# Kernel optimization log

Hardware: AMD Instinct MI355X
Metric: run time of the kernel (lower is better)

## Reference

```python
import jax, jax.numpy as jnp
import numpy as np
from jax import lax


def _shifted(X, k, alpha):
    # alpha * roll(X, -k, 0) + (1 - alpha) * roll(X, -k-1, 0), via gather
    N = X.shape[0]
    idx = (jnp.arange(N) + k) % N
    return alpha * X[idx] + (1.0 - alpha) * X[(idx + 1) % N]


def _all_distances(D_q, D_p, steps):
    # steps: [S] float32 signed step values. Returns [S] mean L2 distances.
    N = D_q.shape[0]
    rows = jnp.arange(N)

    def dist_one(step):
        s = jnp.abs(step)
        k = jnp.floor(s).astype(jnp.int32)          # int(step) of |step|
        alpha = s - k.astype(step.dtype)
        diff = lax.cond(
            step >= 0,
            lambda: _shifted(D_q, k, alpha) - D_p,   # shift query forward
            lambda: D_q - _shifted(D_p, k, alpha),   # shift positive (ref) forward
        )
        norms = jnp.sqrt(jnp.sum(diff * diff, axis=-1))  # [N]
        valid = rows < (N - k)                       # rows [:N - int_step]
        return jnp.sum(jnp.where(valid, norms, 0.0)) / (N - k).astype(norms.dtype)

    def body(carry, step):
        return carry, dist_one(step)

    _, dists = lax.scan(body, None, steps)
    return dists


def setup_inputs() -> dict:
    key = jax.random.key(0)
    k1, k2 = jax.random.split(key)
    N, D = 100000, 256
    return {
        "D_q": jax.random.normal(k1, (N, D), dtype=jnp.float32),
        "D_p": jax.random.normal(k2, (N, D), dtype=jnp.float32),
        "max_step": 60,
        "step_size": 1,
    }


def reference(D_q, D_p, max_step, step_size):
    # Same candidate step schedule as the torch loop (static, built on host).
    steps_np = np.concatenate([
        np.arange(0, max_step, step_size),
        -np.arange(1, max_step + 1, step_size),
    ]).astype(np.float32)
    steps = jnp.asarray(steps_np)                    # [2*max_step/step_size]
    dists = _all_distances(D_q, D_p, steps)
    i = jnp.argmin(dists)
    return steps[i], dists[i]
```

## Files before the change

### kernel.cpp

```cpp
#include <hip/hip_runtime.h>
#include <math.h>


typedef __attribute__((ext_vector_type(8))) __bf16 bf16x8;
typedef __attribute__((ext_vector_type(16))) float f32x16;

#define LDSH 280
#define RING 6
#define MAXS 128
#define NREP 32

__global__ __launch_bounds__(512, 1)
void band_kernel(const float* __restrict__ Q, const float* __restrict__ P,
                 double* __restrict__ ws,
                 const int* __restrict__ msp, const int* __restrict__ ssp,
                 int N, int TS, int nsb) {
  __shared__ __align__(16) unsigned short Bsh[RING * 32 * LDSH];
  __shared__ __align__(16) unsigned short Qsh[2 * 32 * LDSH];
  __shared__ float NpS[RING * 32];
  __shared__ float NqS[2 * 32];
  __shared__ float sums[MAXS];

  const int t = threadIdx.x;
  const int ms = msp[0], ss = ssp[0];
  const int S1 = (ms + ss - 1) / ss;
  const int S = 2 * S1;

  const int T0 = blockIdx.x * nsb;
  int ns = TS - T0; if (ns > nsb) ns = nsb;
  if (ns <= 0) return;

  for (int i = t; i < MAXS; i += 512) sums[i] = 0.f;

  const int srow = t >> 4;
  const int sc = (t & 15) * 4;

  auto issue = [&](const float* __restrict__ base, int tau, float4* r) {
    const int gr = tau * 32 + srow;
    if (gr >= 0 && gr < N) {
      const float* s = base + (size_t)gr * 256 + sc;
      #pragma unroll
      for (int j = 0; j < 4; ++j)
        r[j] = *reinterpret_cast<const float4*>(s + j * 64);
    } else {
      #pragma unroll
      for (int j = 0; j < 4; ++j) r[j] = make_float4(0.f, 0.f, 0.f, 0.f);
    }
  };

  auto commit = [&](unsigned short* dst, float* ndst, int slot, const float4* r) {
    float nrm = 0.f;
    unsigned short* row = dst + slot * 32 * LDSH + srow * LDSH;
    #pragma unroll
    for (int j = 0; j < 4; ++j) {
      const float f0 = r[j].x, f1 = r[j].y, f2 = r[j].z, f3 = r[j].w;
      nrm = fmaf(f0, f0, nrm); nrm = fmaf(f1, f1, nrm);
      nrm = fmaf(f2, f2, nrm); nrm = fmaf(f3, f3, nrm);
      ushort4 h;
      h.x = __builtin_bit_cast(unsigned short, (__bf16)f0);
      h.y = __builtin_bit_cast(unsigned short, (__bf16)f1);
      h.z = __builtin_bit_cast(unsigned short, (__bf16)f2);
      h.w = __builtin_bit_cast(unsigned short, (__bf16)f3);
      *reinterpret_cast<ushort4*>(row + j * 64 + sc) = h;
    }
    nrm += __shfl_xor(nrm, 1); nrm += __shfl_xor(nrm, 2);
    nrm += __shfl_xor(nrm, 4); nrm += __shfl_xor(nrm, 8);
    if ((t & 15) == 0) ndst[slot * 32 + srow] = nrm;
  };

  const int lane = t & 63;
  const int wid = t >> 6;
  const int l31 = lane & 31;
  const int hi = lane >> 5;

  int slotR[16];
  #pragma unroll
  for (int r = 0; r < 16; ++r) {
    int slot = -1;
    if (wid < 5) {
      const int arow = (r & 3) + 8 * (r >> 2) + 4 * hi;
      const int d = arow - l31 - (wid - 2) * 32;
      if (d >= 1) {
        const int k = d - 1;
        if (k < ms && (k % ss) == 0) slot = k / ss;
      } else if (d <= -2) {
        const int kk = -d - 1;
        if (kk <= ms && ((kk - 1) % ss) == 0) slot = S1 + (kk - 1) / ss;
      }
      if (slot >= MAXS) slot = -1;
    }
    slotR[r] = slot;
  }
  float racc[16];
  #pragma unroll
  for (int r = 0; r < 16; ++r) racc[r] = 0.f;

  float4 qA[4], pA[4], qB[4], pB[4];
  {
    float4 u[4], v[4];
    issue(P, T0 - 2, u);
    #pragma unroll
    for (int i = 0; i < 5; ++i) {
      if (i < 4) issue(P, T0 - 1 + i, v);
      commit(Bsh, NpS, (T0 - 2 + i + 12) % RING, u);
      #pragma unroll
      for (int j = 0; j < 4; ++j) u[j] = v[j];
    }
    issue(Q, T0, u);
    commit(Qsh, NqS, T0 & 1, u);
    issue(Q, T0 + 1, qA);
    issue(P, T0 + 3, pA);
  }
  __syncthreads();

  #pragma unroll 1
  for (int s = 0; s < ns; ++s) {
    const int T = T0 + s;
    issue(Q, T + 2, qB);
    issue(P, T + 4, pB);

    if (wid < 5) {
      const int tauW = T - 2 + wid;
      const int slot6 = (tauW + 12) % RING;
      const unsigned short* Ab = &Qsh[(T & 1) * 32 * LDSH + l31 * LDSH + hi * 8];
      const unsigned short* Bb = &Bsh[slot6 * 32 * LDSH + l31 * LDSH + hi * 8];
      f32x16 acc0 = {}, acc1 = {};
      #pragma unroll
      for (int ks = 0; ks < 16; ks += 2) {
        const bf16x8 a0 = *reinterpret_cast<const bf16x8*>(Ab + ks * 16);
        const bf16x8 b0 = *reinterpret_cast<const bf16x8*>(Bb + ks * 16);
        const bf16x8 a1 = *reinterpret_cast<const bf16x8*>(Ab + ks * 16 + 16);
        const bf16x8 b1 = *reinterpret_cast<const bf16x8*>(Bb + ks * 16 + 16);
        acc0 = __builtin_amdgcn_mfma_f32_32x32x16_bf16(a0, b0, acc0, 0, 0, 0);
        acc1 = __builtin_amdgcn_mfma_f32_32x32x16_bf16(a1, b1, acc1, 0, 0, 0);
      }

      const int bcol = tauW * 32 + l31;
      if (bcol >= 0 && bcol < N) {
        const float npW = NpS[slot6 * 32 + l31];
        const int aT = T * 32;
        #pragma unroll
        for (int r = 0; r < 16; ++r) {
          const int arow = (r & 3) + 8 * (r >> 2) + 4 * hi;
          if (slotR[r] >= 0 && (aT + arow) < N) {
            const float n2 = NqS[(T & 1) * 32 + arow] + npW
                             - 2.0f * (acc0[r] + acc1[r]);
            racc[r] += sqrtf(fmaxf(n2, 0.f));
          }
        }
      }
    }

    commit(Qsh, NqS, (T + 1) & 1, qA);
    commit(Bsh, NpS, (T + 3 + 12) % RING, pA);
    #pragma unroll
    for (int j = 0; j < 4; ++j) { qA[j] = qB[j]; pA[j] = pB[j]; }
    __syncthreads();
  }

  #pragma unroll
  for (int r = 0; r < 16; ++r)
    if (slotR[r] >= 0 && racc[r] != 0.f) atomicAdd(&sums[slotR[r]], racc[r]);
  __syncthreads();

  if (t < S && t < MAXS) {
    const float v = sums[t];
    if (v != 0.f)
      unsafeAtomicAdd(&ws[(size_t)(blockIdx.x & (NREP - 1)) * MAXS + t], (double)v);
  }
}

__global__ void corner_kernel(const float* __restrict__ Q, const float* __restrict__ P,
                              double* __restrict__ ws,
                              const int* __restrict__ msp, const int* __restrict__ ssp,
                              int N) {
  const int ms = msp[0], ss = ssp[0];
  const int S1 = (ms + ss - 1) / ss;
  const int S = 2 * S1;
  const int s = blockIdx.x;
  if (s >= S) return;
  int k, qr, pr;
  if (s < S1) { k = s * ss;            qr = 0;           pr = N - (k + 1); }
  else        { k = 1 + (s - S1) * ss; qr = N - (k + 1); pr = 0; }
  const int t = threadIdx.x;
  const float e = Q[(size_t)qr * 256 + t] - P[(size_t)pr * 256 + t];
  float sq = e * e;
  #pragma unroll
  for (int off = 32; off >= 1; off >>= 1) sq += __shfl_down(sq, off);
  __shared__ float red[4];
  if ((t & 63) == 0) red[t >> 6] = sq;
  __syncthreads();
  if (t == 0)
    ws[(size_t)NREP * MAXS + s] = (double)sqrtf(red[0] + red[1] + red[2] + red[3]);
}

__global__ void finalize_kernel(const double* __restrict__ ws, float* __restrict__ out,
                                const int* __restrict__ msp, const int* __restrict__ ssp,
                                int N) {
  __shared__ double dist_sh[MAXS];
  const int t = threadIdx.x;
  const int ms = msp[0], ss = ssp[0];
  const int S1 = (ms + ss - 1) / ss;
  const int S = 2 * S1;
  if (t < S && t < MAXS) {
    double tot = 0.0;
    for (int rep = 0; rep < NREP; ++rep) tot += ws[(size_t)rep * MAXS + t];
    tot += ws[(size_t)NREP * MAXS + t];
    const int k = (t < S1) ? t * ss : 1 + (t - S1) * ss;
    dist_sh[t] = tot / (double)(N - k);
  }
  __syncthreads();
  if (t == 0) {
    int best = 0;
    double bd = dist_sh[0];
    for (int s = 1; s < S && s < MAXS; ++s)
      if (dist_sh[s] < bd) { bd = dist_sh[s]; best = s; }
    const int k = (best < S1) ? best * ss : 1 + (best - S1) * ss;
    out[0] = (best < S1) ? (float)k : -(float)k;
    out[1] = (float)bd;
  }
}

extern "C" void kernel_launch(void* const* d_in, const int* in_sizes, int n_in,
                              void* d_out, int out_size, void* d_ws, size_t ws_size,
                              hipStream_t stream) {
  const float* Q   = (const float*)d_in[0];
  const float* P   = (const float*)d_in[1];
  const int*   msp = (const int*)d_in[2];
  const int*   ssp = (const int*)d_in[3];
  const int N = in_sizes[0] / 256;
  double* ws = (double*)d_ws;

  hipMemsetAsync(d_ws, 0, (size_t)(NREP + 1) * MAXS * sizeof(double), stream);

  const int TS = (N + 31) / 32;
  int nsb = (TS + 249) / 250;
  if (nsb < 1) nsb = 1;
  const int grid = (TS + nsb - 1) / nsb;

  band_kernel<<<grid, 512, 0, stream>>>(Q, P, ws, msp, ssp, N, TS, nsb);
  corner_kernel<<<MAXS, 256, 0, stream>>>(Q, P, ws, msp, ssp, N);
  finalize_kernel<<<1, 128, 0, stream>>>(ws, (float*)d_out, msp, ssp, N);
}
```

Before: 74.31 us.

## Warp-specialize band kernel with producer waves and fold corner kernel into it

Splits each block into 5 MFMA consumer waves and 4 dedicated loader waves that fill the LDS ring, synchronised by packed shared-memory counters with spin-waits instead of a block-wide barrier per step. The corner computation moves into extra blocks of the same launch, which removes one kernel launch. Consumers raise their scheduling priority around the MFMA loop. The aim is to overlap global loads and bf16 conversion with matrix math and to cut barrier stalls and launch overhead. In exchange it adds spin-wait polling, relies on volatile LDS counters with fences for correctness, and caps counter fields at 6-bit and 8-bit widths, which is why nsb is clamped to 60.

Result: faster. 61.87 us (median of 2 runs) (-16.7%).

```diff
diff --git a/kernel.cpp b/kernel.cpp
--- a/kernel.cpp
+++ b/kernel.cpp
@@ -4,82 +4,147 @@
 
 typedef __attribute__((ext_vector_type(8))) __bf16 bf16x8;
 typedef __attribute__((ext_vector_type(16))) float f32x16;
+typedef __attribute__((ext_vector_type(8))) unsigned short us8;
 
 #define LDSH 280
 #define RING 6
 #define MAXS 128
 #define NREP 32
 
-__global__ __launch_bounds__(512, 1)
+__device__ __forceinline__ unsigned short f2bf(float x) {
+  return __builtin_bit_cast(unsigned short, (__bf16)x);
+}
+
+__global__ __launch_bounds__(576, 1)
 void band_kernel(const float* __restrict__ Q, const float* __restrict__ P,
                  double* __restrict__ ws,
                  const int* __restrict__ msp, const int* __restrict__ ssp,
-                 int N, int TS, int nsb) {
+                 int N, int TS, int nsb, int gridB) {
   __shared__ __align__(16) unsigned short Bsh[RING * 32 * LDSH];
   __shared__ __align__(16) unsigned short Qsh[2 * 32 * LDSH];
   __shared__ float NpS[RING * 32];
   __shared__ float NqS[2 * 32];
   __shared__ float sums[MAXS];
+  __shared__ float red[12];
+  __shared__ int packs[2];
 
   const int t = threadIdx.x;
+  const int lane = t & 63;
+  const int wid = t >> 6;
   const int ms = msp[0], ss = ssp[0];
   const int S1 = (ms + ss - 1) / ss;
   const int S = 2 * S1;
 
+  if (blockIdx.x >= gridB) {
+    const int si = blockIdx.x - gridB;
+    if (si >= S) return;
+    int k, qr, pr;
+    if (si < S1) { k = si * ss;            qr = 0;           pr = N - (k + 1); }
+    else         { k = 1 + (si - S1) * ss; qr = N - (k + 1); pr = 0; }
+    float sq = 0.f;
+    if (t < 256) {
+      const float e = Q[(size_t)qr * 256 + t] - P[(size_t)pr * 256 + t];
+      sq = e * e;
+    }
+    #pragma unroll
+    for (int off = 32; off >= 1; off >>= 1) sq += __shfl_xor(sq, off);
+    if (lane == 0) red[wid] = sq;
+    __syncthreads();
+    if (t == 0) {
+      float tot = 0.f;
+      #pragma unroll
+      for (int w = 0; w < 9; ++w) tot += red[w];
+      ws[(size_t)NREP * MAXS + si] = (double)sqrtf(tot);
+    }
+    return;
+  }
+
   const int T0 = blockIdx.x * nsb;
   int ns = TS - T0; if (ns > nsb) ns = nsb;
   if (ns <= 0) return;
 
-  for (int i = t; i < MAXS; i += 512) sums[i] = 0.f;
-
-  const int srow = t >> 4;
-  const int sc = (t & 15) * 4;
-
-  auto issue = [&](const float* __restrict__ base, int tau, float4* r) {
-    const int gr = tau * 32 + srow;
-    if (gr >= 0 && gr < N) {
-      const float* s = base + (size_t)gr * 256 + sc;
+  for (int i = t; i < MAXS; i += 576) sums[i] = 0.f;
+  if (t == 0) { packs[0] = 0; packs[1] = 0; }
+  __syncthreads();
+
+  volatile int* vprod = &packs[0];
+  volatile int* vcons = &packs[1];
+
+  if (wid >= 5) {
+    const int pw = wid - 5;
+    const int rr = pw * 8 + (lane >> 3);
+    const int li = lane & 7;
+
+    float4 vp[8], vq[8];
+
+    auto issueT = [&](const float* __restrict__ base, int tau, float4* v) {
+      const int gr = tau * 32 + rr;
+      if (gr >= 0 && gr < N) {
+        const float* src = base + (size_t)gr * 256 + li * 8;
+        #pragma unroll
+        for (int j = 0; j < 4; ++j) {
+          v[2 * j]     = *reinterpret_cast<const float4*>(src + j * 64);
+          v[2 * j + 1] = *reinterpret_cast<const float4*>(src + j * 64 + 4);
+        }
+      } else {
+        #pragma unroll
+        for (int j = 0; j < 8; ++j) v[j] = make_float4(0.f, 0.f, 0.f, 0.f);
+      }
+    };
+
+    auto commitT = [&](unsigned short* dst, float* ndst, int slot, const float4* v) {
+      float nrm = 0.f;
+      unsigned short* row = dst + slot * 32 * LDSH + rr * LDSH + li * 8;
       #pragma unroll
-      for (int j = 0; j < 4; ++j)
-        r[j] = *reinterpret_cast<const float4*>(s + j * 64);
-    } else {
-      #pragma unroll
-      for (int j = 0; j < 4; ++j) r[j] = make_float4(0.f, 0.f, 0.f, 0.f);
-    }
-  };
-
-  auto commit = [&](unsigned short* dst, float* ndst, int slot, const float4* r) {
-    float nrm = 0.f;
-    unsigned short* row = dst + slot * 32 * LDSH + srow * LDSH;
-    #pragma unroll
-    for (int j = 0; j < 4; ++j) {
-      const float f0 = r[j].x, f1 = r[j].y, f2 = r[j].z, f3 = r[j].w;
-      nrm = fmaf(f0, f0, nrm); nrm = fmaf(f1, f1, nrm);
-      nrm = fmaf(f2, f2, nrm); nrm = fmaf(f3, f3, nrm);
-      ushort4 h;
-      h.x = __builtin_bit_cast(unsigned short, (__bf16)f0);
-      h.y = __builtin_bit_cast(unsigned short, (__bf16)f1);
-      h.z = __builtin_bit_cast(unsigned short, (__bf16)f2);
-      h.w = __builtin_bit_cast(unsigned short, (__bf16)f3);
-      *reinterpret_cast<ushort4*>(row + j * 64 + sc) = h;
-    }
-    nrm += __shfl_xor(nrm, 1); nrm += __shfl_xor(nrm, 2);
-    nrm += __shfl_xor(nrm, 4); nrm += __shfl_xor(nrm, 8);
-    if ((t & 15) == 0) ndst[slot * 32 + srow] = nrm;
-  };
-
-  const int lane = t & 63;
-  const int wid = t >> 6;
-  const int l31 = lane & 31;
-  const int hi = lane >> 5;
-
-  int slotR[16];
-  #pragma unroll
-  for (int r = 0; r < 16; ++r) {
-    int slot = -1;
-    if (wid < 5) {
+      for (int j = 0; j < 4; ++j) {
+        const float f0 = v[2*j].x, f1 = v[2*j].y, f2 = v[2*j].z, f3 = v[2*j].w;
+        const float f4 = v[2*j+1].x, f5 = v[2*j+1].y, f6 = v[2*j+1].z, f7 = v[2*j+1].w;
+        nrm = fmaf(f0, f0, nrm); nrm = fmaf(f1, f1, nrm);
+        nrm = fmaf(f2, f2, nrm); nrm = fmaf(f3, f3, nrm);
+        nrm = fmaf(f4, f4, nrm); nrm = fmaf(f5, f5, nrm);
+        nrm = fmaf(f6, f6, nrm); nrm = fmaf(f7, f7, nrm);
+        us8 h;
+        h[0] = f2bf(f0); h[1] = f2bf(f1); h[2] = f2bf(f2); h[3] = f2bf(f3);
+        h[4] = f2bf(f4); h[5] = f2bf(f5); h[6] = f2bf(f6); h[7] = f2bf(f7);
+        *reinterpret_cast<us8*>(row + j * 64) = h;
+      }
+      nrm += __shfl_xor(nrm, 1);
+      nrm += __shfl_xor(nrm, 2);
+      nrm += __shfl_xor(nrm, 4);
+      if (li == 0) ndst[slot * 32 + rr] = nrm;
+    };
+
+    #pragma unroll 1
+    for (int r = -4; r < ns; ++r) {
+      const int tauP = T0 + r + 2;
+      const bool doQ = (r >= 0);
+      issueT(P, tauP, vp);
+      if (doQ) issueT(Q, T0 + r, vq);
+      const int needc = r - 1;
+      if (needc > 0) {
+        for (;;) {
+          const int v = *vcons;
+          if ((v & 63) >= needc && ((v >> 6) & 63) >= needc &&
+              ((v >> 12) & 63) >= needc && ((v >> 18) & 63) >= needc &&
+              ((v >> 24) & 63) >= needc) break;
+          __builtin_amdgcn_s_sleep(2);
+        }
+      }
+      commitT(Bsh, NpS, (tauP + 12) % RING, vp);
+      if (doQ) commitT(Qsh, NqS, (T0 + r) & 1, vq);
+      __threadfence_block();
+      if (lane == 0) atomicAdd(&packs[0], 1 << (8 * pw));
+    }
+  } else {
+    const int l31 = lane & 31;
+    const int hi = lane >> 5;
+
+    int slotR[16];
+    #pragma unroll
+    for (int r = 0; r < 16; ++r) {
       const int arow = (r & 3) + 8 * (r >> 2) + 4 * hi;
       const int d = arow - l31 - (wid - 2) * 32;
+      int slot = -1;
       if (d >= 1) {
         const int k = d - 1;
         if (k < ms && (k % ss) == 0) slot = k / ss;
@@ -88,43 +153,30 @@
         if (kk <= ms && ((kk - 1) % ss) == 0) slot = S1 + (kk - 1) / ss;
       }
       if (slot >= MAXS) slot = -1;
-    }
-    slotR[r] = slot;
-  }
-  float racc[16];
-  #pragma unroll
-  for (int r = 0; r < 16; ++r) racc[r] = 0.f;
-
-  float4 qA[4], pA[4], qB[4], pB[4];
-  {
-    float4 u[4], v[4];
-    issue(P, T0 - 2, u);
-    #pragma unroll
-    for (int i = 0; i < 5; ++i) {
-      if (i < 4) issue(P, T0 - 1 + i, v);
-      commit(Bsh, NpS, (T0 - 2 + i + 12) % RING, u);
-      #pragma unroll
-      for (int j = 0; j < 4; ++j) u[j] = v[j];
-    }
-    issue(Q, T0, u);
-    commit(Qsh, NqS, T0 & 1, u);
-    issue(Q, T0 + 1, qA);
-    issue(P, T0 + 3, pA);
-  }
-  __syncthreads();
-
-  #pragma unroll 1
-  for (int s = 0; s < ns; ++s) {
-    const int T = T0 + s;
-    issue(Q, T + 2, qB);
-    issue(P, T + 4, pB);
-
-    if (wid < 5) {
+      slotR[r] = slot;
+    }
+    float racc[16];
+    #pragma unroll
+    for (int r = 0; r < 16; ++r) racc[r] = 0.f;
+
+    #pragma unroll 1
+    for (int s = 0; s < ns; ++s) {
+      const int T = T0 + s;
+      const int need = s + 5;
+      for (;;) {
+        const int v = *vprod;
+        if ((v & 255) >= need && ((v >> 8) & 255) >= need &&
+            ((v >> 16) & 255) >= need && ((v >> 24) & 255) >= need) break;
+        __builtin_amdgcn_s_sleep(2);
+      }
+      __threadfence_block();
+
       const int tauW = T - 2 + wid;
       const int slot6 = (tauW + 12) % RING;
       const unsigned short* Ab = &Qsh[(T & 1) * 32 * LDSH + l31 * LDSH + hi * 8];
       const unsigned short* Bb = &Bsh[slot6 * 32 * LDSH + l31 * LDSH + hi * 8];
       f32x16 acc0 = {}, acc1 = {};
+      __builtin_amdgcn_s_setprio(1);
       #pragma unroll
       for (int ks = 0; ks < 16; ks += 2) {
         const bf16x8 a0 = *reinterpret_cast<const bf16x8*>(Ab + ks * 16);
@@ -134,6 +186,7 @@
         acc0 = __builtin_amdgcn_mfma_f32_32x32x16_bf16(a0, b0, acc0, 0, 0, 0);
         acc1 = __builtin_amdgcn_mfma_f32_32x32x16_bf16(a1, b1, acc1, 0, 0, 0);
       }
+      __builtin_amdgcn_s_setprio(0);
 
       const int bcol = tauW * 32 + l31;
       if (bcol >= 0 && bcol < N) {
@@ -149,49 +202,22 @@
           }
         }
       }
-    }
-
-    commit(Qsh, NqS, (T + 1) & 1, qA);
-    commit(Bsh, NpS, (T + 3 + 12) % RING, pA);
-    #pragma unroll
-    for (int j = 0; j < 4; ++j) { qA[j] = qB[j]; pA[j] = pB[j]; }
-    __syncthreads();
-  }
-
-  #pragma unroll
-  for (int r = 0; r < 16; ++r)
-    if (slotR[r] >= 0 && racc[r] != 0.f) atomicAdd(&sums[slotR[r]], racc[r]);
+
+      __threadfence_block();
+      if (lane == 0) atomicAdd(&packs[1], 1 << (6 * wid));
+    }
+
+    #pragma unroll
+    for (int r = 0; r < 16; ++r)
+      if (slotR[r] >= 0 && racc[r] != 0.f) atomicAdd(&sums[slotR[r]], racc[r]);
+  }
+
   __syncthreads();
-
   if (t < S && t < MAXS) {
     const float v = sums[t];
     if (v != 0.f)
       unsafeAtomicAdd(&ws[(size_t)(blockIdx.x & (NREP - 1)) * MAXS + t], (double)v);
   }
-}
-
-__global__ void corner_kernel(const float* __restrict__ Q, const float* __restrict__ P,
-                              double* __restrict__ ws,
-                              const int* __restrict__ msp, const int* __restrict__ ssp,
-                              int N) {
-  const int ms = msp[0], ss = ssp[0];
-  const int S1 = (ms + ss - 1) / ss;
-  const int S = 2 * S1;
-  const int s = blockIdx.x;
-  if (s >= S) return;
-  int k, qr, pr;
-  if (s < S1) { k = s * ss;            qr = 0;           pr = N - (k + 1); }
-  else        { k = 1 + (s - S1) * ss; qr = N - (k + 1); pr = 0; }
-  const int t = threadIdx.x;
-  const float e = Q[(size_t)qr * 256 + t] - P[(size_t)pr * 256 + t];
-  float sq = e * e;
-  #pragma unroll
-  for (int off = 32; off >= 1; off >>= 1) sq += __shfl_down(sq, off);
-  __shared__ float red[4];
-  if ((t & 63) == 0) red[t >> 6] = sq;
-  __syncthreads();
-  if (t == 0)
-    ws[(size_t)NREP * MAXS + s] = (double)sqrtf(red[0] + red[1] + red[2] + red[3]);
 }
 
 __global__ void finalize_kernel(const double* __restrict__ ws, float* __restrict__ out,
@@ -236,9 +262,10 @@
   const int TS = (N + 31) / 32;
   int nsb = (TS + 249) / 250;
   if (nsb < 1) nsb = 1;
-  const int grid = (TS + nsb - 1) / nsb;
-
-  band_kernel<<<grid, 512, 0, stream>>>(Q, P, ws, msp, ssp, N, TS, nsb);
-  corner_kernel<<<MAXS, 256, 0, stream>>>(Q, P, ws, msp, ssp, N);
+  if (nsb > 60) nsb = 60;
+  const int gridB = (TS + nsb - 1) / nsb;
+
+  band_kernel<<<gridB + MAXS, 576, 0, stream>>>(Q, P, ws, msp, ssp,
+                                                N, TS, nsb, gridB);
   finalize_kernel<<<1, 128, 0, stream>>>(ws, (float*)d_out, msp, ssp, N);
 }
```
